# Performance work log

Hardware: AMD Instinct MI355X
Metric: run time of the kernel (lower is better)

## Reference

```python
import jax, jax.numpy as jnp
import numpy as np

B, N_ANG, LX, LY, LZ = 2, 120, 128, 128, 128


def _rotate_z(vol, phi):
    """Rotate vol [B,Lx,Ly,Lz] by phi radians (counterclockwise) in the (x,y)
    plane about the grid center, bilinear interpolation, zero padding.
    Mirrors pytomography's rotate_detector_z (bilinear grid-sample rotate)."""
    Lx, Ly = vol.shape[1], vol.shape[2]
    dt = vol.dtype
    cx = (Lx - 1) / 2.0
    cy = (Ly - 1) / 2.0
    xs = jnp.arange(Lx, dtype=dt) - cx
    ys = jnp.arange(Ly, dtype=dt) - cy
    X, Y = jnp.meshgrid(xs, ys, indexing="ij")  # [Lx,Ly]
    c, s = jnp.cos(phi), jnp.sin(phi)
    # inverse rotation maps each output pixel to its source location
    sx = c * X + s * Y + cx
    sy = -s * X + c * Y + cy
    x0 = jnp.floor(sx)
    y0 = jnp.floor(sy)
    wx = (sx - x0)[None, :, :, None]
    wy = (sy - y0)[None, :, :, None]
    x0i = x0.astype(jnp.int32)
    y0i = y0.astype(jnp.int32)

    def gather(xi, yi):
        valid = (xi >= 0) & (xi < Lx) & (yi >= 0) & (yi < Ly)
        xic = jnp.clip(xi, 0, Lx - 1)
        yic = jnp.clip(yi, 0, Ly - 1)
        v = vol[:, xic, yic, :]  # [B,Lx,Ly,Lz]
        return v * valid.astype(dt)[None, :, :, None]

    v00 = gather(x0i, y0i)
    v01 = gather(x0i, y0i + 1)
    v10 = gather(x0i + 1, y0i)
    v11 = gather(x0i + 1, y0i + 1)
    return (v00 * (1 - wx) * (1 - wy) + v01 * (1 - wx) * wy
            + v10 * wx * (1 - wy) + v11 * wx * wy)


def setup_inputs() -> dict:
    key = jax.random.key(0)
    image = jax.random.uniform(key, (B, N_ANG, LY, LZ), dtype=jnp.float32)
    angles = jnp.linspace(0.0, 360.0, N_ANG, endpoint=False).astype(jnp.float32)
    return {"image": image, "angles": angles}


def reference(image, angles, delta=1e-11):
    # image: [B, N_angles, Lr, Lz]; angles in degrees.
    Bn, Na, Lr, Lz = image.shape
    Lx = Ly = Lr
    dt = image.dtype
    phis = -jnp.deg2rad(angles).astype(dt)  # negative=True -> back-rotation

    def step(carry, inp):
        obj_acc, norm_acc = carry
        proj, phi = inp  # proj: [B, Lr, Lz]
        # image[:, i].unsqueeze(1) * ones([B, Lx, Ly, Lz]): broadcast along x
        obj_i = jnp.broadcast_to(proj[:, None, :, :], (Bn, Lx, Ly, Lz))
        norm_i = jnp.ones((Bn, Lx, Ly, Lz), dt)
        obj_acc = obj_acc + _rotate_z(obj_i, phi)
        norm_acc = norm_acc + _rotate_z(norm_i, phi)
        return (obj_acc, norm_acc), None

    init = (jnp.zeros((Bn, Lx, Ly, Lz), dt), jnp.zeros((Bn, Lx, Ly, Lz), dt))
    (obj, norm), _ = jax.lax.scan(step, init, (jnp.swapaxes(image, 0, 1), phis))
    return obj / (norm + jnp.asarray(delta, dt))
```

## Files before the change

kernel.cpp:

```cpp
#include <hip/hip_runtime.h>

namespace {

constexpr int L           = 128;
constexpr int NANG        = 120;
constexpr int SLICE_BYTES = L * L * 4;
constexpr int ROW_BYTES   = L * 4;

typedef __fp16 f16x2 __attribute__((ext_vector_type(2)));
typedef __fp16 f16x4 __attribute__((ext_vector_type(4)));
typedef float  f32x4 __attribute__((ext_vector_type(4)));

__global__ __launch_bounds__(512, 4) void bp_kernel(
    const float* __restrict__ image,
    const float* __restrict__ angles,
    float* __restrict__ out)
{
    __shared__ alignas(16) uint2 wtab[NANG * 32];
    __shared__ float2   acs[NANG];
    __shared__ unsigned arlo[NANG];
    __shared__ alignas(16) float nrmtab[32];

    const int tid = threadIdx.x;
    const int yb  = blockIdx.x * 4;
    const int xb  = blockIdx.y * 8;
    const float cx = (L - 1) * 0.5f;

    if (tid < NANG) {
        const float phi = -angles[tid] * 0.017453292519943295f;
        float s, c;
        sincosf(phi, &s, &c);
        const float X0 = (float)xb - cx,       X1 = (float)(xb + 7) - cx;
        const float Y0 = (float)yb - cx,       Y1 = (float)(yb + 3) - cx;
        const float a00 = -s * X0 + c * Y0 + cx;
        const float a01 = -s * X0 + c * Y1 + cx;
        const float a10 = -s * X1 + c * Y0 + cx;
        const float a11 = -s * X1 + c * Y1 + cx;
        const float symin = fminf(fminf(a00, a01), fminf(a10, a11));
        acs[tid]  = make_float2(c, s);
        arlo[tid] = (unsigned)min(max((int)floorf(symin) - 1, 0), 116);
    }
    if (tid < 32) nrmtab[tid] = 0.f;
    __syncthreads();

    for (int e = tid; e < 32 * NANG; e += 512) {
        const int p = e / NANG;
        const int a = e - p * NANG;
        const float2 cs = acs[a];
        const int rlo = (int)arlo[a];
        const float X = (float)(xb + (p >> 2)) - cx;
        const float Y = (float)(yb + (p & 3)) - cx;
        const float sx =  cs.x * X + cs.y * Y + cx;
        const float sy = -cs.y * X + cs.x * Y + cx;
        const float x0f = floorf(sx), y0f = floorf(sy);
        const float wx = sx - x0f,    wy = sy - y0f;
        const int x0 = (int)x0f, y0 = (int)y0f;
        const float mx0 = (x0 >= 0  && x0 <  L)     ? 1.f : 0.f;
        const float mx1 = (x0 >= -1 && x0 <= L - 2) ? 1.f : 0.f;
        const float my0 = (y0 >= 0  && y0 <  L)     ? 1.f : 0.f;
        const float my1 = (y0 >= -1 && y0 <= L - 2) ? 1.f : 0.f;
        const float A   = (1.f - wx) * mx0 + wx * mx1;
        float w0f = (1.f - wy) * my0 * A;
        float w1f = wy * my1 * A;
        const int y0c = min(max(y0, 0), L - 1);
        const int y1c = min(max(y0 + 1, 0), L - 1);
        const int s0  = min(max(y0c - rlo, 0), 11);
        const int s1  = min(max(y1c - rlo, 0), 11);
        if (s0 == s1) { w0f += w1f; w1f = 0.f; }
        f16x2 wh = __builtin_amdgcn_cvt_pkrtz(w0f, w1f);
        uint2 ent;
        ent.x = *reinterpret_cast<unsigned*>(&wh);
        ent.y = (unsigned)s0;
        wtab[a * 32 + p] = ent;
        atomicAdd(&nrmtab[p], w0f + w1f);
    }
    __syncthreads();

    const int wave  = tid >> 6;
    const int lane  = tid & 63;
    const int quad  = lane >> 4;
    const int lhalf = lane & 15;
    const int b     = wave & 1;
    const int zq2   = wave >> 1;
    const char* __restrict__ imgc = (const char*)image;

    const unsigned bbase_s = __builtin_amdgcn_readfirstlane((unsigned)(b * NANG) * SLICE_BYTES);
    const unsigned zoff0   = (unsigned)((zq2 * 2) * 16 + lhalf) * 4u;
    const int quad4 = (quad == 3) ? 0 : (quad * 4);
    unsigned qz[4];
#pragma unroll
    for (int j = 0; j < 4; ++j) qz[j] = (unsigned)(quad4 + j) * ROW_BYTES + zoff0;

    f32x4 acc[2][2] = {};

    auto build_af = [&](uint2 e) -> f16x4 {
        const unsigned s0 = e.y;
        const unsigned t  = s0 & 3u;
        const int      q0 = (int)(s0 >> 2);
        const unsigned long long W = (unsigned long long)e.x << (t * 16u);
        const unsigned spill = (t == 3u) ? (e.x >> 16) : 0u;
        const unsigned long long af64 =
            (quad == q0) ? W : ((quad == q0 + 1) ? (unsigned long long)spill : 0ull);
        union { unsigned long long u; f16x4 v; } c; c.u = af64; return c.v;
    };

    auto read_tab = [&](int pr, uint2* tA, uint2* tB, unsigned* rl) {
        const int a = 2 * pr;
        tA[0] = wtab[a * 32 + lhalf];
        tB[0] = wtab[a * 32 + 16 + lhalf];
        tA[1] = wtab[(a + 1) * 32 + lhalf];
        tB[1] = wtab[(a + 1) * 32 + 16 + lhalf];
        rl[0] = __builtin_amdgcn_readfirstlane(arlo[a]);
        rl[1] = __builtin_amdgcn_readfirstlane(arlo[a + 1]);
    };
    auto issue2 = [&](int pr, const unsigned* rl, float* r) {
        const int a = 2 * pr;
#pragma unroll
        for (int u = 0; u < 2; ++u) {
            const char* pa = imgc + (bbase_s + ((unsigned)(a + u) << 16) + (rl[u] << 9));
#pragma unroll
            for (int j = 0; j < 4; ++j) {
                r[u * 8 + j * 2 + 0] = *(const float*)(pa + qz[j]);
                r[u * 8 + j * 2 + 1] = *(const float*)(pa + qz[j] + 64);
            }
        }
    };
    auto compute = [&](uint2 eA, uint2 eB, const float* r) {
        const f16x4 af0 = build_af(eA);
        const f16x4 af1 = build_af(eB);
#pragma unroll
        for (int i = 0; i < 2; ++i) {
            const f16x2 h01 = __builtin_amdgcn_cvt_pkrtz(r[0 + i], r[2 + i]);
            const f16x2 h23 = __builtin_amdgcn_cvt_pkrtz(r[4 + i], r[6 + i]);
            const f16x4 bf = {h01.x, h01.y, h23.x, h23.y};
            acc[0][i] = __builtin_amdgcn_mfma_f32_16x16x16f16(af0, bf, acc[0][i], 0, 0, 0);
            acc[1][i] = __builtin_amdgcn_mfma_f32_16x16x16f16(af1, bf, acc[1][i], 0, 0, 0);
        }
    };

    uint2 A0[2], B0[2], A1[2], B1[2], A2[2], B2[2];
    unsigned R0[2], R1[2], R2[2];
    float rb0[16], rb1[16], rb2[16];

    read_tab(0, A0, B0, R0); issue2(0, R0, rb0);
    read_tab(1, A1, B1, R1); issue2(1, R1, rb1);

    for (int p = 0; p < 60; p += 3) {
        if (p + 2 < 60) { read_tab(p + 2, A2, B2, R2); issue2(p + 2, R2, rb2); }
        compute(A0[0], B0[0], rb0);
        compute(A0[1], B0[1], rb0 + 8);
        if (p + 3 < 60) { read_tab(p + 3, A0, B0, R0); issue2(p + 3, R0, rb0); }
        compute(A1[0], B1[0], rb1);
        compute(A1[1], B1[1], rb1 + 8);
        if (p + 4 < 60) { read_tab(p + 4, A1, B1, R1); issue2(p + 4, R1, rb1); }
        compute(A2[0], B2[0], rb2);
        compute(A2[1], B2[1], rb2 + 8);
    }

#pragma unroll
    for (int mt = 0; mt < 2; ++mt) {
        const float4 nrm4 = *(const float4*)&nrmtab[mt * 16 + quad * 4];
        const float iv[4] = { 1.f / (nrm4.x + 1e-11f), 1.f / (nrm4.y + 1e-11f),
                              1.f / (nrm4.z + 1e-11f), 1.f / (nrm4.w + 1e-11f) };
#pragma unroll
        for (int i = 0; i < 2; ++i) {
            const int z = (zq2 * 2 + i) * 16 + lhalf;
#pragma unroll
            for (int r = 0; r < 4; ++r) {
                const int p = mt * 16 + quad * 4 + r;
                const int x = xb + (p >> 2);
                const int y = yb + (p & 3);
                out[(((size_t)(b * L + x)) * L + y) * L + z] = acc[mt][i][r] * iv[r];
            }
        }
    }
}

}

extern "C" void kernel_launch(void* const* d_in, const int* in_sizes, int n_in,
                              void* d_out, int out_size, void* d_ws, size_t ws_size,
                              hipStream_t stream) {
    const float* image  = (const float*)d_in[0];
    const float* angles = (const float*)d_in[1];
    float* out = (float*)d_out;
    (void)in_sizes; (void)n_in; (void)out_size; (void)d_ws; (void)ws_size;

    dim3 grid(L / 4, L / 8);
    bp_kernel<<<grid, 512, 0, stream>>>(image, angles, out);
}
```

Before: 126.0 us.

## Shrink tile to 4x4 points, pack two angles per MFMA, prebuild A-fragments

Each block now covers a 4x4 (x,y) tile instead of 4x8, which doubles the grid to 1024 blocks, remapped through a swizzled 1D index. Each MFMA K dimension now spans two angles, with 8 source rows per angle instead of 12. The fp16 A-fragment words are fully precomputed into shared memory, so the main loop does a single 64-bit LDS read per lane instead of rebuilding them with selects. Image loads become float2 vectors and output stores are float2, the norm atomics are reduced per thread first, and launch bounds ask for 8 blocks per CU. The aim is more parallelism and fewer per-iteration instructions, at the cost of more redundant table setup per output point and narrower row windows per angle.

```diff
diff --git a/kernel.cpp b/kernel.cpp
--- a/kernel.cpp
+++ b/kernel.cpp
@@ -6,173 +6,157 @@
 constexpr int NANG        = 120;
 constexpr int SLICE_BYTES = L * L * 4;
 constexpr int ROW_BYTES   = L * 4;
+constexpr int NPTS        = 16;
 
 typedef __fp16 f16x2 __attribute__((ext_vector_type(2)));
 typedef __fp16 f16x4 __attribute__((ext_vector_type(4)));
 typedef float  f32x4 __attribute__((ext_vector_type(4)));
 
-__global__ __launch_bounds__(512, 4) void bp_kernel(
+__global__ __launch_bounds__(512, 8) void bp_kernel(
     const float* __restrict__ image,
     const float* __restrict__ angles,
     float* __restrict__ out)
 {
-    __shared__ alignas(16) uint2 wtab[NANG * 32];
+    __shared__ alignas(16) unsigned long long aftab[NANG * 2 * NPTS];
     __shared__ float2   acs[NANG];
-    __shared__ unsigned arlo[NANG];
-    __shared__ alignas(16) float nrmtab[32];
+    __shared__ unsigned arloB[NANG];
+    __shared__ alignas(16) float nrmtab[NPTS];
 
     const int tid = threadIdx.x;
-    const int yb  = blockIdx.x * 4;
-    const int xb  = blockIdx.y * 8;
+    const int swz = ((int)blockIdx.x & 7) * 128 + ((int)blockIdx.x >> 3);
+    const int yb  = (swz & 31) * 4;
+    const int xb  = (swz >> 5) * 4;
     const float cx = (L - 1) * 0.5f;
 
     if (tid < NANG) {
         const float phi = -angles[tid] * 0.017453292519943295f;
         float s, c;
         sincosf(phi, &s, &c);
-        const float X0 = (float)xb - cx,       X1 = (float)(xb + 7) - cx;
-        const float Y0 = (float)yb - cx,       Y1 = (float)(yb + 3) - cx;
+        const float X0 = (float)xb - cx,  X1 = (float)(xb + 3) - cx;
+        const float Y0 = (float)yb - cx,  Y1 = (float)(yb + 3) - cx;
         const float a00 = -s * X0 + c * Y0 + cx;
         const float a01 = -s * X0 + c * Y1 + cx;
         const float a10 = -s * X1 + c * Y0 + cx;
         const float a11 = -s * X1 + c * Y1 + cx;
         const float symin = fminf(fminf(a00, a01), fminf(a10, a11));
-        acs[tid]  = make_float2(c, s);
-        arlo[tid] = (unsigned)min(max((int)floorf(symin) - 1, 0), 116);
+        acs[tid]   = make_float2(c, s);
+        arloB[tid] = (unsigned)min(max((int)floorf(symin) - 1, 0), 120) << 9;
     }
-    if (tid < 32) nrmtab[tid] = 0.f;
+    if (tid < NPTS) nrmtab[tid] = 0.f;
     __syncthreads();
 
-    for (int e = tid; e < 32 * NANG; e += 512) {
-        const int p = e / NANG;
-        const int a = e - p * NANG;
-        const float2 cs = acs[a];
-        const int rlo = (int)arlo[a];
-        const float X = (float)(xb + (p >> 2)) - cx;
-        const float Y = (float)(yb + (p & 3)) - cx;
-        const float sx =  cs.x * X + cs.y * Y + cx;
-        const float sy = -cs.y * X + cs.x * Y + cx;
-        const float x0f = floorf(sx), y0f = floorf(sy);
-        const float wx = sx - x0f,    wy = sy - y0f;
-        const int x0 = (int)x0f, y0 = (int)y0f;
-        const float mx0 = (x0 >= 0  && x0 <  L)     ? 1.f : 0.f;
-        const float mx1 = (x0 >= -1 && x0 <= L - 2) ? 1.f : 0.f;
-        const float my0 = (y0 >= 0  && y0 <  L)     ? 1.f : 0.f;
-        const float my1 = (y0 >= -1 && y0 <= L - 2) ? 1.f : 0.f;
-        const float A   = (1.f - wx) * mx0 + wx * mx1;
-        float w0f = (1.f - wy) * my0 * A;
-        float w1f = wy * my1 * A;
-        const int y0c = min(max(y0, 0), L - 1);
-        const int y1c = min(max(y0 + 1, 0), L - 1);
-        const int s0  = min(max(y0c - rlo, 0), 11);
-        const int s1  = min(max(y1c - rlo, 0), 11);
-        if (s0 == s1) { w0f += w1f; w1f = 0.f; }
-        f16x2 wh = __builtin_amdgcn_cvt_pkrtz(w0f, w1f);
-        uint2 ent;
-        ent.x = *reinterpret_cast<unsigned*>(&wh);
-        ent.y = (unsigned)s0;
-        wtab[a * 32 + p] = ent;
-        atomicAdd(&nrmtab[p], w0f + w1f);
+    float wsum = 0.f;
+#pragma unroll
+    for (int k = 0; k < 4; ++k) {
+        const int e = tid + k * 512;
+        if (e < NANG * NPTS) {
+            const int p = e & 15;
+            const int a = e >> 4;
+            const float2 cs = acs[a];
+            const int rlo = (int)(arloB[a] >> 9);
+            const float X = (float)(xb + (p >> 2)) - cx;
+            const float Y = (float)(yb + (p & 3)) - cx;
+            const float sx =  cs.x * X + cs.y * Y + cx;
+            const float sy = -cs.y * X + cs.x * Y + cx;
+            const float x0f = floorf(sx), y0f = floorf(sy);
+            const float wx = sx - x0f,    wy = sy - y0f;
+            const int x0 = (int)x0f, y0 = (int)y0f;
+            const float mx0 = (x0 >= 0  && x0 <  L)     ? 1.f : 0.f;
+            const float mx1 = (x0 >= -1 && x0 <= L - 2) ? 1.f : 0.f;
+            const float my0 = (y0 >= 0  && y0 <  L)     ? 1.f : 0.f;
+            const float my1 = (y0 >= -1 && y0 <= L - 2) ? 1.f : 0.f;
+            const float A   = (1.f - wx) * mx0 + wx * mx1;
+            float w0f = (1.f - wy) * my0 * A;
+            float w1f = wy * my1 * A;
+            const int y0c = min(max(y0, 0), L - 1);
+            const int y1c = min(max(y0 + 1, 0), L - 1);
+            const int s0  = min(max(y0c - rlo, 0), 7);
+            const int s1  = min(max(y1c - rlo, 0), 7);
+            if (s0 == s1) { w0f += w1f; w1f = 0.f; }
+            f16x2 wh = __builtin_amdgcn_cvt_pkrtz(w0f, w1f);
+            const unsigned wbits = *reinterpret_cast<unsigned*>(&wh);
+            const unsigned t  = (unsigned)s0 & 3u;
+            const int      q0 = s0 >> 2;
+            const unsigned long long W = (unsigned long long)wbits << (t * 16u);
+            const unsigned long long spill =
+                (t == 3u) ? (unsigned long long)(wbits >> 16) : 0ull;
+            aftab[a * 32 + p]      = (q0 == 0) ? W : 0ull;
+            aftab[a * 32 + 16 + p] = (q0 == 1) ? W : spill;
+            wsum += w0f + w1f;
+        }
     }
+    atomicAdd(&nrmtab[tid & 15], wsum);
     __syncthreads();
 
     const int wave  = tid >> 6;
     const int lane  = tid & 63;
     const int quad  = lane >> 4;
     const int lhalf = lane & 15;
+    const int sel   = quad >> 1;
+    const int lq    = quad & 1;
     const int b     = wave & 1;
     const int zq2   = wave >> 1;
     const char* __restrict__ imgc = (const char*)image;
 
     const unsigned bbase_s = __builtin_amdgcn_readfirstlane((unsigned)(b * NANG) * SLICE_BYTES);
-    const unsigned zoff0   = (unsigned)((zq2 * 2) * 16 + lhalf) * 4u;
-    const int quad4 = (quad == 3) ? 0 : (quad * 4);
-    unsigned qz[4];
+    const unsigned voffc = (unsigned)sel * (unsigned)SLICE_BYTES
+                         + (unsigned)(lq * 4) * ROW_BYTES
+                         + (unsigned)(zq2 * 32 + 2 * lhalf) * 4u;
+
+    f32x4 acc[2] = {};
+
+    auto read_af = [&](int pr) -> unsigned long long {
+        return aftab[pr * 64 + lane];
+    };
+    auto read_rl = [&](int pr) -> unsigned {
+        return arloB[2 * pr + sel];
+    };
+    auto issue = [&](int pr, unsigned rlB, float2* r) {
+        const char* pa = imgc + (bbase_s + ((unsigned)(2 * pr) << 16));
+        const unsigned voff = voffc + rlB;
 #pragma unroll
-    for (int j = 0; j < 4; ++j) qz[j] = (unsigned)(quad4 + j) * ROW_BYTES + zoff0;
-
-    f32x4 acc[2][2] = {};
-
-    auto build_af = [&](uint2 e) -> f16x4 {
-        const unsigned s0 = e.y;
-        const unsigned t  = s0 & 3u;
-        const int      q0 = (int)(s0 >> 2);
-        const unsigned long long W = (unsigned long long)e.x << (t * 16u);
-        const unsigned spill = (t == 3u) ? (e.x >> 16) : 0u;
-        const unsigned long long af64 =
-            (quad == q0) ? W : ((quad == q0 + 1) ? (unsigned long long)spill : 0ull);
-        union { unsigned long long u; f16x4 v; } c; c.u = af64; return c.v;
+        for (int j = 0; j < 4; ++j)
+            r[j] = *(const float2*)(pa + (voff + (unsigned)(j * ROW_BYTES)));
+    };
+    auto compute = [&](unsigned long long afu, const float2* r) {
+        union { unsigned long long u; f16x4 v; } c; c.u = afu;
+        const f16x2 h0a = __builtin_amdgcn_cvt_pkrtz(r[0].x, r[1].x);
+        const f16x2 h0b = __builtin_amdgcn_cvt_pkrtz(r[2].x, r[3].x);
+        const f16x2 h1a = __builtin_amdgcn_cvt_pkrtz(r[0].y, r[1].y);
+        const f16x2 h1b = __builtin_amdgcn_cvt_pkrtz(r[2].y, r[3].y);
+        const f16x4 bf0 = {h0a.x, h0a.y, h0b.x, h0b.y};
+        const f16x4 bf1 = {h1a.x, h1a.y, h1b.x, h1b.y};
+        acc[0] = __builtin_amdgcn_mfma_f32_16x16x16f16(c.v, bf0, acc[0], 0, 0, 0);
+        acc[1] = __builtin_amdgcn_mfma_f32_16x16x16f16(c.v, bf1, acc[1], 0, 0, 0);
     };
 
-    auto read_tab = [&](int pr, uint2* tA, uint2* tB, unsigned* rl) {
-        const int a = 2 * pr;
-        tA[0] = wtab[a * 32 + lhalf];
-        tB[0] = wtab[a * 32 + 16 + lhalf];
-        tA[1] = wtab[(a + 1) * 32 + lhalf];
-        tB[1] = wtab[(a + 1) * 32 + 16 + lhalf];
-        rl[0] = __builtin_amdgcn_readfirstlane(arlo[a]);
-        rl[1] = __builtin_amdgcn_readfirstlane(arlo[a + 1]);
-    };
-    auto issue2 = [&](int pr, const unsigned* rl, float* r) {
-        const int a = 2 * pr;
-#pragma unroll
-        for (int u = 0; u < 2; ++u) {
-            const char* pa = imgc + (bbase_s + ((unsigned)(a + u) << 16) + (rl[u] << 9));
-#pragma unroll
-            for (int j = 0; j < 4; ++j) {
-                r[u * 8 + j * 2 + 0] = *(const float*)(pa + qz[j]);
-                r[u * 8 + j * 2 + 1] = *(const float*)(pa + qz[j] + 64);
-            }
-        }
-    };
-    auto compute = [&](uint2 eA, uint2 eB, const float* r) {
-        const f16x4 af0 = build_af(eA);
-        const f16x4 af1 = build_af(eB);
-#pragma unroll
-        for (int i = 0; i < 2; ++i) {
-            const f16x2 h01 = __builtin_amdgcn_cvt_pkrtz(r[0 + i], r[2 + i]);
-            const f16x2 h23 = __builtin_amdgcn_cvt_pkrtz(r[4 + i], r[6 + i]);
-            const f16x4 bf = {h01.x, h01.y, h23.x, h23.y};
-            acc[0][i] = __builtin_amdgcn_mfma_f32_16x16x16f16(af0, bf, acc[0][i], 0, 0, 0);
-            acc[1][i] = __builtin_amdgcn_mfma_f32_16x16x16f16(af1, bf, acc[1][i], 0, 0, 0);
-        }
-    };
+    unsigned long long af0, af1, af2;
+    unsigned rl0, rl1, rl2;
+    float2 rb0[4], rb1[4], rb2[4];
 
-    uint2 A0[2], B0[2], A1[2], B1[2], A2[2], B2[2];
-    unsigned R0[2], R1[2], R2[2];
-    float rb0[16], rb1[16], rb2[16];
-
-    read_tab(0, A0, B0, R0); issue2(0, R0, rb0);
-    read_tab(1, A1, B1, R1); issue2(1, R1, rb1);
+    af0 = read_af(0); rl0 = read_rl(0); issue(0, rl0, rb0);
+    af1 = read_af(1); rl1 = read_rl(1); issue(1, rl1, rb1);
 
     for (int p = 0; p < 60; p += 3) {
-        if (p + 2 < 60) { read_tab(p + 2, A2, B2, R2); issue2(p + 2, R2, rb2); }
-        compute(A0[0], B0[0], rb0);
-        compute(A0[1], B0[1], rb0 + 8);
-        if (p + 3 < 60) { read_tab(p + 3, A0, B0, R0); issue2(p + 3, R0, rb0); }
-        compute(A1[0], B1[0], rb1);
-        compute(A1[1], B1[1], rb1 + 8);
-        if (p + 4 < 60) { read_tab(p + 4, A1, B1, R1); issue2(p + 4, R1, rb1); }
-        compute(A2[0], B2[0], rb2);
-        compute(A2[1], B2[1], rb2 + 8);
+        if (p + 2 < 60) { af2 = read_af(p + 2); rl2 = read_rl(p + 2); issue(p + 2, rl2, rb2); }
+        compute(af0, rb0);
+        if (p + 3 < 60) { af0 = read_af(p + 3); rl0 = read_rl(p + 3); issue(p + 3, rl0, rb0); }
+        compute(af1, rb1);
+        if (p + 4 < 60) { af1 = read_af(p + 4); rl1 = read_rl(p + 4); issue(p + 4, rl1, rb1); }
+        compute(af2, rb2);
     }
 
+    const float4 nrm4 = *(const float4*)&nrmtab[quad * 4];
+    const float iv[4] = { 1.f / (nrm4.x + 1e-11f), 1.f / (nrm4.y + 1e-11f),
+                          1.f / (nrm4.z + 1e-11f), 1.f / (nrm4.w + 1e-11f) };
+    const int zb = zq2 * 32 + 2 * lhalf;
 #pragma unroll
-    for (int mt = 0; mt < 2; ++mt) {
-        const float4 nrm4 = *(const float4*)&nrmtab[mt * 16 + quad * 4];
-        const float iv[4] = { 1.f / (nrm4.x + 1e-11f), 1.f / (nrm4.y + 1e-11f),
-                              1.f / (nrm4.z + 1e-11f), 1.f / (nrm4.w + 1e-11f) };
-#pragma unroll
-        for (int i = 0; i < 2; ++i) {
-            const int z = (zq2 * 2 + i) * 16 + lhalf;
-#pragma unroll
-            for (int r = 0; r < 4; ++r) {
-                const int p = mt * 16 + quad * 4 + r;
-                const int x = xb + (p >> 2);
-                const int y = yb + (p & 3);
-                out[(((size_t)(b * L + x)) * L + y) * L + z] = acc[mt][i][r] * iv[r];
-            }
-        }
+    for (int r = 0; r < 4; ++r) {
+        const int pnt = quad * 4 + r;
+        const int x = xb + (pnt >> 2);
+        const int y = yb + (pnt & 3);
+        const float2 o = make_float2(acc[0][r] * iv[r], acc[1][r] * iv[r]);
+        *reinterpret_cast<float2*>(&out[(((size_t)(b * L + x)) * L + y) * L + zb]) = o;
     }
 }
 
@@ -186,6 +170,6 @@
     float* out = (float*)d_out;
     (void)in_sizes; (void)n_in; (void)out_size; (void)d_ws; (void)ws_size;
 
-    dim3 grid(L / 4, L / 8);
+    dim3 grid(1024);
     bp_kernel<<<grid, 512, 0, stream>>>(image, angles, out);
 }
```

New measurement: 122.7 us. -2.6%, faster.
